# Kernel tuning notes

Hardware: AMD Instinct MI355X
Metric: run time of the kernel (lower is better)

The kernel has to match this reference:

```python
import jax, jax.numpy as jnp
import numpy as np

NUM_HEADS = 8
DIM = 192  # target_dim = min(channels_list)
CHANNELS = [192, 384, 768]
SIZES = [(32, 32), (16, 16), (8, 8)]
BATCH = 4


def conv1x1(x, w, b):
    # x: [B,C,H,W], w: [O,C,1,1], b: [O]
    y = jnp.einsum('bchw,oc->bohw', x, w[:, :, 0, 0])
    return y + b[None, :, None, None]


def cross_attention(x, ctx, wq, wkv, wp, bp):
    # x: [B,N,C] queries, ctx: [B,M,C] key/value source
    B, N, C = x.shape
    M = ctx.shape[1]
    h = NUM_HEADS
    d = C // h
    scale = d ** -0.5
    q = (x @ wq.T).reshape(B, N, h, d).transpose(0, 2, 1, 3)          # [B,h,N,d]
    kv = ctx @ wkv.T                                                   # [B,M,2C]
    k = kv[..., :C].reshape(B, M, h, d).transpose(0, 2, 1, 3)          # [B,h,M,d]
    v = kv[..., C:].reshape(B, M, h, d).transpose(0, 2, 1, 3)          # [B,h,M,d]
    attn = jax.nn.softmax(jnp.einsum('bhnd,bhmd->bhnm', q, k) * scale, axis=-1)
    o = jnp.einsum('bhnm,bhmd->bhnd', attn, v)
    o = o.transpose(0, 2, 1, 3).reshape(B, N, C)
    return o @ wp.T + bp


def setup_inputs() -> dict:
    key = jax.random.key(0)
    ks = iter(jax.random.split(key, 64))
    s = 0.02
    inp = {}
    for i, (c, (H, W)) in enumerate(zip(CHANNELS, SIZES)):
        inp[f'f{i}'] = jax.random.normal(next(ks), (BATCH, c, H, W), dtype=jnp.float32)
    # input projections (scale 0 has c == target_dim -> Identity, no params)
    for i in (1, 2):
        c = CHANNELS[i]
        inp[f'proj{i}_w'] = jax.random.normal(next(ks), (DIM, c, 1, 1), dtype=jnp.float32) * s
        inp[f'proj{i}_b'] = jnp.zeros((DIM,), dtype=jnp.float32)
    # cross-attention params per scale (qkv_bias=False; proj has bias)
    for i in range(3):
        inp[f'q{i}_w'] = jax.random.normal(next(ks), (DIM, DIM), dtype=jnp.float32) * s
        inp[f'kv{i}_w'] = jax.random.normal(next(ks), (2 * DIM, DIM), dtype=jnp.float32) * s
        inp[f'pr{i}_w'] = jax.random.normal(next(ks), (DIM, DIM), dtype=jnp.float32) * s
        inp[f'pr{i}_b'] = jnp.zeros((DIM,), dtype=jnp.float32)
    # output projections back to each channel count
    for i, c in enumerate(CHANNELS):
        inp[f'out{i}_w'] = jax.random.normal(next(ks), (c, DIM, 1, 1), dtype=jnp.float32) * s
        inp[f'out{i}_b'] = jnp.zeros((c,), dtype=jnp.float32)
    return inp


def _forward(f0, f1, f2,
             proj1_w, proj1_b, proj2_w, proj2_b,
             q0_w, kv0_w, pr0_w, pr0_b,
             q1_w, kv1_w, pr1_w, pr1_b,
             q2_w, kv2_w, pr2_w, pr2_b,
             out0_w, out0_b, out1_w, out1_b, out2_w, out2_b):
    projected = [
        f0,  # Identity (channels == target_dim)
        conv1x1(f1, proj1_w, proj1_b),
        conv1x1(f2, proj2_w, proj2_b),
    ]
    attn_params = [
        (q0_w, kv0_w, pr0_w, pr0_b),
        (q1_w, kv1_w, pr1_w, pr1_b),
        (q2_w, kv2_w, pr2_w, pr2_b),
    ]
    out_params = [(out0_w, out0_b), (out1_w, out1_b), (out2_w, out2_b)]
    outputs = []
    for i in range(3):
        feat = projected[i]
        B, C, H, W = feat.shape
        x = feat.reshape(B, C, H * W).transpose(0, 2, 1)  # [B,N,C]
        ctxs = []
        for j in range(3):
            if j != i:
                r = jax.image.resize(projected[j], (B, C, H, W), method='bilinear', antialias=False)
                ctxs.append(r.reshape(B, C, H * W).transpose(0, 2, 1))
        ctx = jnp.concatenate(ctxs, axis=1)  # [B,M,C]
        enh = cross_attention(x, ctx, *attn_params[i])
        enh = enh.transpose(0, 2, 1).reshape(B, C, H, W) + feat
        outputs.append(conv1x1(enh, *out_params[i]))
    return tuple(outputs)


def reference(f0, f1, f2,
              proj1_w, proj1_b, proj2_w, proj2_b,
              q0_w, kv0_w, pr0_w, pr0_b,
              q1_w, kv1_w, pr1_w, pr1_b,
              q2_w, kv2_w, pr2_w, pr2_b,
              out0_w, out0_b, out1_w, out1_b, out2_w, out2_b):
    return _forward(f0, f1, f2,
                    proj1_w, proj1_b, proj2_w, proj2_b,
                    q0_w, kv0_w, pr0_w, pr0_b,
                    q1_w, kv1_w, pr1_w, pr1_b,
                    q2_w, kv2_w, pr2_w, pr2_b,
                    out0_w, out0_b, out1_w, out1_b, out2_w, out2_b)
```

## Files before the change

kernel.cpp:

```cpp
#include <hip/hip_runtime.h>
#include <math.h>

#define BB 4
#define DIM 192
#define HEADS 8
#define HD 24

typedef __attribute__((ext_vector_type(8))) short short8v;
typedef __attribute__((ext_vector_type(4))) short short4v;
typedef __attribute__((ext_vector_type(4))) float f32x4;
typedef __attribute__((ext_vector_type(4))) unsigned uint4v;

__device__ __forceinline__ short f2bf(float f) {
  unsigned u = __builtin_bit_cast(unsigned, f);
  u += 0x7FFF + ((u >> 16) & 1);
  return (short)(u >> 16);
}
__device__ __forceinline__ unsigned pk2(float a, float b) {
  return (unsigned)(unsigned short)f2bf(a) | ((unsigned)(unsigned short)f2bf(b) << 16);
}
__device__ __forceinline__ float bf2f(unsigned u16) {
  return __builtin_bit_cast(float, u16 << 16);
}
__device__ __forceinline__ void gl_lds16(const void* g, void* l) {
  __builtin_amdgcn_global_load_lds(
      (const __attribute__((address_space(1))) unsigned int*)g,
      (__attribute__((address_space(3))) unsigned int*)l, 16, 0, 0);
}
__device__ __forceinline__ int xcd_swz(int bid, int nwg) {
  int q = nwg >> 3, r = nwg & 7;
  int xcd = bid & 7, idx = bid >> 3;
  return (xcd < r) ? (xcd * (q + 1) + idx) : (r * (q + 1) + (xcd - r) * q + idx);
}

struct PJob {
  int type;
  const float* s0; const float* s1; const float* s2;
  void* dst;
  int P0, P1v;
  int t_begin, t_end;
};
struct PJobs { PJob j[20]; };

__global__ __launch_bounds__(256) void prep_k(PJobs jobs, int nj) {
  int tid = blockIdx.x * 256 + threadIdx.x;
  for (int ji = 0; ji < 20; ++ji) {
    if (ji >= nj) return;
    PJob g = jobs.j[ji];
    if (tid < g.t_begin || tid >= g.t_end) continue;
    int t = tid - g.t_begin;
    if (g.type == 0) {
      float4 v = *(const float4*)&g.s0[(size_t)t * 4];
      uint2 u = {pk2(v.x, v.y), pk2(v.z, v.w)};
      *(uint2*)&((short*)g.dst)[(size_t)t * 4] = u;
    } else if (g.type == 1) {
      int X = g.P0, C = g.P1v, C8 = C >> 3;
      int x = t % X, c8 = (t / X) % C8, b = t / (X * C8);
      const float* s = g.s0 + ((size_t)b * C + c8 * 8) * X + x;
      unsigned h[8];
#pragma unroll
      for (int j = 0; j < 8; ++j) h[j] = (unsigned)(unsigned short)f2bf(s[(size_t)j * X]);
      uint4 u = {h[0] | (h[1] << 16), h[2] | (h[3] << 16), h[4] | (h[5] << 16), h[6] | (h[7] << 16)};
      *(uint4*)&((short*)g.dst)[((size_t)b * X + x) * C + c8 * 8] = u;
    } else if (g.type == 2) {
      int o = t;
      const float* w = g.s0 + (size_t)o * 192;
      float acc = g.s2[o];
      for (int k = 0; k < 192; ++k) acc += w[k] * g.s1[k];
      ((float*)g.dst)[o] = acc;
    } else {
      int c4 = t % 48, o = t / 48;
      const float* w = g.s0 + (size_t)o * 192;
      float a0 = 0, a1 = 0, a2 = 0, a3 = 0;
      for (int k = 0; k < 192; ++k) {
        float wv = w[k];
        float4 pv = *(const float4*)&g.s1[(size_t)k * 192 + c4 * 4];
        a0 += wv * pv.x; a1 += wv * pv.y; a2 += wv * pv.z; a3 += wv * pv.w;
      }
      uint2 u = {pk2(a0, a1), pk2(a2, a3)};
      *(uint2*)&((short*)g.dst)[(size_t)o * 192 + c4 * 4] = u;
    }
    return;
  }
}

struct MJob {
  const short* A; const short* W; const float* bias; const float* T;
  void* out;
  int K, nOT, mode, tokPerB;
  float scale;
  int blk_begin, blk_end;
};
struct MJobs { MJob j[10]; };

__global__ __launch_bounds__(256) void mgemm_k(MJobs jobs, int nj, int nwg) {
  __shared__ short Asl[64 * 192];
  __shared__ short Wsl[64 * 192];
  int blk = xcd_swz(blockIdx.x, nwg);
  for (int ji = 0; ji < 10; ++ji) {
    if (ji >= nj) return;
    MJob g = jobs.j[ji];
    if (blk < g.blk_begin || blk >= g.blk_end) continue;
    int lb = blk - g.blk_begin;
    int ot = lb % g.nOT, tt = lb / g.nOT;
    int t0 = tt * 64, o0 = ot * 64;
    int tid = threadIdx.x, wv = tid >> 6, lane = tid & 63, c = lane & 15, qi = lane >> 4;
    const int K = g.K;
    int rowK[6];
#pragma unroll
    for (int i = 0; i < 6; ++i) {
      int o16 = i * 256 + tid;
      int row = o16 / 24, ch = o16 - row * 24;
      rowK[i] = row * K + ((ch ^ (row & 7)) << 3);
    }
    const short* Ab = g.A + (size_t)t0 * K;
    const short* Wb = g.W + (size_t)o0 * K;
    f32x4 acc[4];
#pragma unroll
    for (int jj = 0; jj < 4; ++jj) acc[jj] = (f32x4){0.f, 0.f, 0.f, 0.f};
    int nkc = K / 192;
    int swz = c & 7;
    for (int kc = 0; kc < nkc; ++kc) {
      if (kc) __syncthreads();
      int kco = kc * 192;
#pragma unroll
      for (int i = 0; i < 6; ++i) gl_lds16(Ab + rowK[i] + kco, &Asl[(i * 256 + wv * 64) * 8]);
#pragma unroll
      for (int i = 0; i < 6; ++i) gl_lds16(Wb + rowK[i] + kco, &Wsl[(i * 256 + wv * 64) * 8]);
      asm volatile("s_waitcnt vmcnt(0)" ::: "memory");
      __syncthreads();
      const short* Lb = (g.mode == 0) ? Wsl : Asl;
      const short* Rb = (g.mode == 0) ? Asl : Wsl;
      int lrow = wv * 16 + c;
#pragma unroll
      for (int ks = 0; ks < 6; ++ks) {
        int chx = ((ks * 4 + qi) ^ swz) << 3;
        short8v lf = *(const short8v*)&Lb[lrow * 192 + chx];
#pragma unroll
        for (int jj = 0; jj < 4; ++jj) {
          short8v rf = *(const short8v*)&Rb[(jj * 16 + c) * 192 + chx];
          acc[jj] = __builtin_amdgcn_mfma_f32_16x16x32_bf16(lf, rf, acc[jj], 0, 0, 0);
        }
      }
    }
    int OST = g.nOT * 64;
    if (g.mode == 0) {
      int ob = o0 + wv * 16 + (qi << 2);
      float4 bv = {0.f, 0.f, 0.f, 0.f};
      if (g.bias) bv = *(const float4*)&g.bias[ob];
      float s = g.scale;
      short* op = (short*)g.out;
#pragma unroll
      for (int jj = 0; jj < 4; ++jj) {
        size_t tok = t0 + jj * 16 + c;
        uint2 u = {pk2(acc[jj][0] * s + bv.x, acc[jj][1] * s + bv.y),
                   pk2(acc[jj][2] * s + bv.z, acc[jj][3] * s + bv.w)};
        *(uint2*)&op[tok * OST + ob] = u;
      }
    } else {
      int tokb = t0 + wv * 16;
      int b = tokb / g.tokPerB;
      int nl = tokb - b * g.tokPerB + (qi << 2);
#pragma unroll
      for (int jj = 0; jj < 4; ++jj) {
        int o = o0 + jj * 16 + c;
        size_t idx = ((size_t)b * OST + o) * g.tokPerB + nl;
        if (g.mode == 1) {
          uint2 u = {pk2(acc[jj][0], acc[jj][1]), pk2(acc[jj][2], acc[jj][3])};
          *(uint2*)&((short*)g.out)[idx] = u;
        } else if (g.mode == 2) {
          float4 tv = *(const float4*)&g.T[idx];
          float4 ov = {acc[jj][0] + tv.x, acc[jj][1] + tv.y, acc[jj][2] + tv.z, acc[jj][3] + tv.w};
          *(float4*)&((float*)g.out)[idx] = ov;
        } else {
          float bvv = g.bias ? g.bias[o] : 0.f;
          float4 ov = {acc[jj][0] + bvv, acc[jj][1] + bvv, acc[jj][2] + bvv, acc[jj][3] + bvv};
          *(float4*)&((float*)g.out)[idx] = ov;
        }
      }
    }
    return;
  }
}

struct RJob {
  const short* src;
  short* dst;
  int Hs, Ws, Wd, Mtot;
  float ry, rx;
  int t_begin, t_end;
};
struct RJobs { RJob j[6]; };

__global__ __launch_bounds__(256) void resize_k(RJobs jobs) {
  int tid = blockIdx.x * 256 + threadIdx.x;
  for (int ji = 0; ji < 6; ++ji) {
    RJob g = jobs.j[ji];
    if (tid < g.t_begin || tid >= g.t_end) continue;
    int t = tid - g.t_begin;
    int c8 = t % 24;
    int rest = t / 24;
    int HWd = g.Wd * g.Wd;
    int n = rest % HWd, b = rest / HWd;
    int y = n / g.Wd, x = n % g.Wd;
    float fy = (y + 0.5f) * g.ry - 0.5f;
    float fx = (x + 0.5f) * g.rx - 0.5f;
    int y0 = (int)floorf(fy), x0 = (int)floorf(fx);
    float wy = fy - (float)y0, wx = fx - (float)x0;
    int Hs = g.Hs, Ws = g.Ws;
    int y0c = min(max(y0, 0), Hs - 1), y1c = min(max(y0 + 1, 0), Hs - 1);
    int x0c = min(max(x0, 0), Ws - 1), x1c = min(max(x0 + 1, 0), Ws - 1);
    size_t sb = (size_t)b * Hs * Ws;
    const short* sp = g.src;
    uint4 u00 = *(const uint4*)&sp[(sb + y0c * Ws + x0c) * 192 + c8 * 8];
    uint4 u01 = *(const uint4*)&sp[(sb + y0c * Ws + x1c) * 192 + c8 * 8];
    uint4 u10 = *(const uint4*)&sp[(sb + y1c * Ws + x0c) * 192 + c8 * 8];
    uint4 u11 = *(const uint4*)&sp[(sb + y1c * Ws + x1c) * 192 + c8 * 8];
    float w00 = (1.f - wy) * (1.f - wx), w01 = (1.f - wy) * wx;
    float w10 = wy * (1.f - wx), w11 = wy * wx;
    unsigned a[4], bq[4], cq[4], dq[4];
    a[0]=u00.x; a[1]=u00.y; a[2]=u00.z; a[3]=u00.w;
    bq[0]=u01.x; bq[1]=u01.y; bq[2]=u01.z; bq[3]=u01.w;
    cq[0]=u10.x; cq[1]=u10.y; cq[2]=u10.z; cq[3]=u10.w;
    dq[0]=u11.x; dq[1]=u11.y; dq[2]=u11.z; dq[3]=u11.w;
    unsigned r[4];
#pragma unroll
    for (int k = 0; k < 4; ++k) {
      float lo = w00 * bf2f(a[k] & 0xffff) + w01 * bf2f(bq[k] & 0xffff) +
                 w10 * bf2f(cq[k] & 0xffff) + w11 * bf2f(dq[k] & 0xffff);
      float hi = w00 * bf2f(a[k] >> 16) + w01 * bf2f(bq[k] >> 16) +
                 w10 * bf2f(cq[k] >> 16) + w11 * bf2f(dq[k] >> 16);
      r[k] = pk2(lo, hi);
    }
    uint4 u = {r[0], r[1], r[2], r[3]};
    *(uint4*)&g.dst[((size_t)b * g.Mtot + n) * 192 + c8 * 8] = u;
    return;
  }
}

struct AJob {
  const short* q;
  const short* K;
  const short* V;
  short* o;
  int N, M;
  int blk_begin, blk_end;
};
struct AJobs { AJob j[3]; };

__global__ __launch_bounds__(256) void attn_k(AJobs jobs, int cpx) {
  __shared__ __align__(16) short LDSbuf[2][7432];
  int bid = blockIdx.x;
  int blk = (bid & 7) * cpx + (bid >> 3);
  int tidx = threadIdx.x;
  if (tidx < 4) {
    ((int*)LDSbuf[0])[1536 + tidx] = 0;
    ((int*)LDSbuf[1])[1536 + tidx] = 0;
  }
  if (tidx < 64) {
    ((int*)LDSbuf[0])[3172 + tidx] = 0x3F803F80;
    ((int*)LDSbuf[1])[3172 + tidx] = 0x3F803F80;
  }
  for (int ji = 0; ji < 3; ++ji) {
    AJob g = jobs.j[ji];
    if (blk < g.blk_begin || blk >= g.blk_end) continue;
    int lb = blk - g.blk_begin;
    const int N = g.N, M = g.M;
    int nch = N >> 6;
    int bh = lb / nch, ct = lb % nch;
    int b = bh >> 3, h = bh & 7;
    int wv = tidx >> 6, lane = tidx & 63;
    int c = lane & 15, qi = lane >> 4;
    int nw0 = (ct << 6) + (wv << 4);

    const short* Kg = g.K + (size_t)b * M * 192 + h * 24;
    const short* Vg = g.V + ((size_t)b * 192 + h * 24) * M;

    const short* gp[4];
    int gstr[4], loff[4];
    bool val[4];
#pragma unroll
    for (int i = 0; i < 4; ++i) {
      int s = tidx + (i << 8);
      val[i] = (s < 792);
      if (s < 384) {
        int row = s / 3, part = s - row * 3;
        gp[i] = Kg + row * 192 + part * 8;
        gstr[i] = 128 * 192;
        loff[i] = s * 8;
      } else {
        int v = s - 384;
        int row = v / 17, col = v - row * 17;
        int colc = (col < 16) ? col : 0;
        gp[i] = val[i] ? (Vg + (size_t)row * M + colc * 8) : Vg;
        gstr[i] = 128;
        loff[i] = 3080 + v * 8;
      }
    }

    short8v qf = *(const short8v*)&g.q[((size_t)b * N + nw0 + c) * 192 + h * 24 + (qi << 3)];
    if (qi == 3) {
#pragma unroll
      for (int j = 0; j < 8; ++j) qf[j] = 0;
    }

    f32x4 of0 = {0.f, 0.f, 0.f, 0.f}, of1 = {0.f, 0.f, 0.f, 0.f};
    const f32x4 zf = {0.f, 0.f, 0.f, 0.f};

#pragma unroll
    for (int i = 0; i < 4; ++i)
      if (val[i]) { gl_lds16(gp[i], &LDSbuf[0][loff[i]]); gp[i] += gstr[i]; }

    int nt = M >> 7;
    int cur = 0;
    for (int t = 0; t < nt; ++t) {
      asm volatile("s_waitcnt vmcnt(0)" ::: "memory");
      __syncthreads();
      if (t + 1 < nt) {
#pragma unroll
        for (int i = 0; i < 4; ++i)
          if (val[i]) { gl_lds16(gp[i], &LDSbuf[cur ^ 1][loff[i]]); gp[i] += gstr[i]; }
      }
      const short* Kl = LDSbuf[cur];
      const short* Vl = LDSbuf[cur] + 3080;
      f32x4 sr[8];
#pragma unroll
      for (int jj = 0; jj < 8; ++jj) {
        short8v kb = *(const short8v*)&Kl[(c + 16 * jj) * 24 + (qi << 3)];
        sr[jj] = __builtin_amdgcn_mfma_f32_16x16x32_bf16(kb, qf, zf, 0, 0, 0);
      }
      unsigned pk[8][2];
#pragma unroll
      for (int jj = 0; jj < 8; ++jj) {
        pk[jj][0] = pk2(__expf(sr[jj][0]), __expf(sr[jj][1]));
        pk[jj][1] = pk2(__expf(sr[jj][2]), __expf(sr[jj][3]));
      }
#pragma unroll
      for (int ks = 0; ks < 4; ++ks) {
        uint4v pu = {pk[2 * ks][0], pk[2 * ks][1], pk[2 * ks + 1][0], pk[2 * ks + 1][1]};
        short8v pa = __builtin_bit_cast(short8v, pu);
        int vb0 = c * 136 + ks * 32 + (qi << 2);
        int vb1 = (16 + c) * 136 + ks * 32 + (qi << 2);
        short4v l0 = *(const short4v*)&Vl[vb0];
        short4v h0 = *(const short4v*)&Vl[vb0 + 16];
        short4v l1 = *(const short4v*)&Vl[vb1];
        short4v h1 = *(const short4v*)&Vl[vb1 + 16];
        short8v v0, v1;
#pragma unroll
        for (int j2 = 0; j2 < 4; ++j2) {
          v0[j2] = l0[j2]; v0[4 + j2] = h0[j2];
          v1[j2] = l1[j2]; v1[4 + j2] = h1[j2];
        }
        of0 = __builtin_amdgcn_mfma_f32_16x16x32_bf16(pa, v0, of0, 0, 0, 0);
        of1 = __builtin_amdgcn_mfma_f32_16x16x32_bf16(pa, v1, of1, 0, 0, 0);
      }
      cur ^= 1;
    }
    float ls[4];
#pragma unroll
    for (int r = 0; r < 4; ++r) ls[r] = __shfl(of1[r], (qi << 4) + 8);
#pragma unroll
    for (int r = 0; r < 4; ++r) {
      float inv = 1.f / ls[r];
      int n = nw0 + (qi << 2) + r;
      short* op = g.o + ((size_t)b * N + n) * 192 + h * 24;
      op[c] = f2bf(of0[r] * inv);
      if (c < 8) op[16 + c] = f2bf(of1[r] * inv);
    }
    return;
  }
}

extern "C" void kernel_launch(void* const* d_in, const int* in_sizes, int n_in,
                              void* d_out, int out_size, void* d_ws, size_t ws_size,
                              hipStream_t stream) {
  (void)in_sizes; (void)n_in; (void)out_size; (void)ws_size;
  const float* f0 = (const float*)d_in[0];
  const float* f1 = (const float*)d_in[1];
  const float* f2 = (const float*)d_in[2];
  const float* p1w = (const float*)d_in[3];
  const float* p1b = (const float*)d_in[4];
  const float* p2w = (const float*)d_in[5];
  const float* p2b = (const float*)d_in[6];
  const float* qw[3]  = {(const float*)d_in[7],  (const float*)d_in[11], (const float*)d_in[15]};
  const float* kvw[3] = {(const float*)d_in[8],  (const float*)d_in[12], (const float*)d_in[16]};
  const float* prw[3] = {(const float*)d_in[9],  (const float*)d_in[13], (const float*)d_in[17]};
  const float* prb[3] = {(const float*)d_in[10], (const float*)d_in[14], (const float*)d_in[18]};
  const float* ow[3]  = {(const float*)d_in[19], (const float*)d_in[21], (const float*)d_in[23]};
  const float* ob[3]  = {(const float*)d_in[20], (const float*)d_in[22], (const float*)d_in[24]};

  char* ws = (char*)d_ws;
  short* x0    = (short*)(ws + 0);
  short* x1in  = (short*)(ws + 1572864);
  short* x2in  = (short*)(ws + 2359296);
  short* P1    = (short*)(ws + 2752512);
  short* P2    = (short*)(ws + 3145728);
  short* ctx0  = (short*)(ws + 3244032);
  short* ctx1  = (short*)(ws + 6389760);
  short* ctx2  = (short*)(ws + 7176192);
  short* qb    = (short*)(ws + 7372800);
  short* Kb    = (short*)(ws + 9437184);
  short* Vb    = (short*)(ws + 13565952);
  short* attb  = (short*)(ws + 17694720);
  float* T0    = (float*)(ws + 19759104);
  float* T1    = (float*)(ws + 22904832);
  float* T2    = (float*)(ws + 24477696);
  short* W2b   = (short*)(ws + 25264128);
  short* wcvt  = (short*)(ws + 25780224);
  float* bfin  = (float*)(ws + 27402240);

  short* p1w_b = wcvt;
  short* p2w_b = wcvt + 73728;
  short* qw_b[3]  = {wcvt + 221184, wcvt + 258048, wcvt + 294912};
  short* kvw_b[3] = {wcvt + 331776, wcvt + 405504, wcvt + 479232};
  short* ow_b[3]  = {wcvt + 552960, wcvt + 589824, wcvt + 663552};
  short* W2_b[3]  = {W2b, W2b + 36864, W2b + 110592};
  short* qs[3]  = {qb, qb + 786432, qb + 983040};
  short* Ks[3]  = {Kb, Kb + 1572864, Kb + 1966080};
  short* Vs[3]  = {Vb, Vb + 1572864, Vb + 1966080};
  short* atts[3] = {attb, attb + 786432, attb + 983040};
  float* out0 = (float*)d_out;
  float* outp[3] = {out0, out0 + 786432, out0 + 1179648};

  const int Ns[3] = {1024, 256, 64};
  const int Ms[3] = {2048, 512, 128};
  const float qsc = 0.20412414523193154f;

  {
    PJobs js{};
    int t0 = 0, n = 0;
    auto add = [&](PJob j, int tc) { j.t_begin = t0; j.t_end = t0 + tc; js.j[n++] = j; t0 += tc; };
    add({0, p1w, nullptr, nullptr, p1w_b, 0, 0, 0, 0}, 18432);
    add({0, p2w, nullptr, nullptr, p2w_b, 0, 0, 0, 0}, 36864);
    for (int i = 0; i < 3; ++i) add({0, qw[i], nullptr, nullptr, qw_b[i], 0, 0, 0, 0}, 9216);
    for (int i = 0; i < 3; ++i) add({0, kvw[i], nullptr, nullptr, kvw_b[i], 0, 0, 0, 0}, 18432);
    add({0, ow[0], nullptr, nullptr, ow_b[0], 0, 0, 0, 0}, 9216);
    add({0, ow[1], nullptr, nullptr, ow_b[1], 0, 0, 0, 0}, 18432);
    add({0, ow[2], nullptr, nullptr, ow_b[2], 0, 0, 0, 0}, 36864);
    add({1, f0, nullptr, nullptr, x0, 1024, 192, 0, 0}, 98304);
    add({1, f1, nullptr, nullptr, x1in, 256, 384, 0, 0}, 49152);
    add({1, f2, nullptr, nullptr, x2in, 64, 768, 0, 0}, 24576);
    add({2, ow[0], prb[0], ob[0], bfin, 0, 0, 0, 0}, 192);
    add({2, ow[1], prb[1], ob[1], bfin + 192, 0, 0, 0, 0}, 384);
    add({2, ow[2], prb[2], ob[2], bfin + 576, 0, 0, 0, 0}, 768);
    add({3, ow[0], prw[0], nullptr, W2_b[0], 0, 0, 0, 0}, 9216);
    add({3, ow[1], prw[1], nullptr, W2_b[1], 0, 0, 0, 0}, 18432);
    add({3, ow[2], prw[2], nullptr, W2_b[2], 0, 0, 0, 0}, 36864);
    hipLaunchKernelGGL(prep_k, dim3((t0 + 255) / 256), dim3(256), 0, stream, js, n);
  }
  {
    MJobs js{};
    int b0 = 0, n = 0;
    auto add = [&](MJob j, int nb) { j.blk_begin = b0; j.blk_end = b0 + nb; js.j[n++] = j; b0 += nb; };
    add({x1in, p1w_b, p1b, nullptr, P1, 384, 3, 0, 0, 1.f, 0, 0}, 16 * 3);
    add({x2in, p2w_b, p2b, nullptr, P2, 768, 3, 0, 0, 1.f, 0, 0}, 4 * 3);
    add({x0, qw_b[0], nullptr, nullptr, qs[0], 192, 3, 0, 0, qsc, 0, 0}, 64 * 3);
    add({x0, ow_b[0], bfin, nullptr, T0, 192, 3, 3, 1024, 1.f, 0, 0}, 64 * 3);
    hipLaunchKernelGGL(mgemm_k, dim3(b0), dim3(256), 0, stream, js, n, b0);
  }
  {
    RJobs js{};
    int t0 = 0, n = 0;
    auto add = [&](RJob j, int tc) { j.t_begin = t0; j.t_end = t0 + tc; js.j[n++] = j; t0 += tc; };
    add({P1, ctx0, 16, 16, 32, 2048, 0.5f, 0.5f, 0, 0}, 98304);
    add({P2, ctx0 + 1024 * 192, 8, 8, 32, 2048, 0.25f, 0.25f, 0, 0}, 98304);
    add({x0, ctx1, 32, 32, 16, 512, 2.f, 2.f, 0, 0}, 24576);
    add({P2, ctx1 + 256 * 192, 8, 8, 16, 512, 0.5f, 0.5f, 0, 0}, 24576);
    add({x0, ctx2, 32, 32, 8, 128, 4.f, 4.f, 0, 0}, 6144);
    add({P1, ctx2 + 64 * 192, 16, 16, 8, 128, 2.f, 2.f, 0, 0}, 6144);
    hipLaunchKernelGGL(resize_k, dim3(t0 / 256), dim3(256), 0, stream, js);
  }
  {
    MJobs js{};
    int b0 = 0, n = 0;
    auto add = [&](MJob j, int nb) { j.blk_begin = b0; j.blk_end = b0 + nb; js.j[n++] = j; b0 += nb; };
    add({P1, qw_b[1], nullptr, nullptr, qs[1], 192, 3, 0, 0, qsc, 0, 0}, 16 * 3);
    add({P2, qw_b[2], nullptr, nullptr, qs[2], 192, 3, 0, 0, qsc, 0, 0}, 4 * 3);
    add({ctx0, kvw_b[0], nullptr, nullptr, Ks[0], 192, 3, 0, 0, 1.f, 0, 0}, 128 * 3);
    add({ctx1, kvw_b[1], nullptr, nullptr, Ks[1], 192, 3, 0, 0, 1.f, 0, 0}, 32 * 3);
    add({ctx2, kvw_b[2], nullptr, nullptr, Ks[2], 192, 3, 0, 0, 1.f, 0, 0}, 8 * 3);
    add({ctx0, kvw_b[0] + 36864, nullptr, nullptr, Vs[0], 192, 3, 1, 2048, 1.f, 0, 0}, 128 * 3);
    add({ctx1, kvw_b[1] + 36864, nullptr, nullptr, Vs[1], 192, 3, 1, 512, 1.f, 0, 0}, 32 * 3);
    add({ctx2, kvw_b[2] + 36864, nullptr, nullptr, Vs[2], 192, 3, 1, 128, 1.f, 0, 0}, 8 * 3);
    add({P1, ow_b[1], bfin + 192, nullptr, T1, 192, 6, 3, 256, 1.f, 0, 0}, 16 * 6);
    add({P2, ow_b[2], bfin + 576, nullptr, T2, 192, 12, 3, 64, 1.f, 0, 0}, 4 * 12);
    hipLaunchKernelGGL(mgemm_k, dim3(b0), dim3(256), 0, stream, js, n, b0);
  }
  {
    AJobs js{};
    int b0 = 0;
    for (int i = 0; i < 3; ++i) {
      int nb = BB * HEADS * (Ns[i] / 64);
      js.j[i] = {qs[i], Ks[i], Vs[i], atts[i], Ns[i], Ms[i], b0, b0 + nb};
      b0 += nb;
    }
    hipLaunchKernelGGL(attn_k, dim3(b0), dim3(256), 0, stream, js, b0 / 8);
  }
  {
    MJobs js{};
    int b0 = 0, n = 0;
    auto add = [&](MJob j, int nb) { j.blk_begin = b0; j.blk_end = b0 + nb; js.j[n++] = j; b0 += nb; };
    add({atts[0], W2_b[0], nullptr, T0, outp[0], 192, 3, 2, 1024, 1.f, 0, 0}, 64 * 3);
    add({atts[1], W2_b[1], nullptr, T1, outp[1], 192, 6, 2, 256, 1.f, 0, 0}, 16 * 6);
    add({atts[2], W2_b[2], nullptr, T2, outp[2], 192, 12, 2, 64, 1.f, 0, 0}, 4 * 12);
    hipLaunchKernelGGL(mgemm_k, dim3(b0), dim3(256), 0, stream, js, n, b0);
  }
}
```

Baseline: 89.52 us.

## Triple-buffer attention loads, pre-permute V layout, and fold weight product into MFMA GEMM

The attention kernel moves from double to triple buffering. It waits with a partial vmcnt so two tiles stay in flight, and it raises wave priority around the MFMA sections. The V output in mode 1 is written with a permuted token order, so attention can load each V fragment with one 16-byte LDS read instead of two 8-byte reads plus a shuffle. The fused out-projection times proj-weight product now runs as a bf16 MFMA GEMM job after transposing prw in prep, replacing the scalar fp32 loop. This adds a third LDS buffer, which may lower occupancy, and the weight product is now computed from bf16 inputs.

```diff
diff --git a/kernel.cpp b/kernel.cpp
--- a/kernel.cpp
+++ b/kernel.cpp
@@ -62,23 +62,12 @@
       for (int j = 0; j < 8; ++j) h[j] = (unsigned)(unsigned short)f2bf(s[(size_t)j * X]);
       uint4 u = {h[0] | (h[1] << 16), h[2] | (h[3] << 16), h[4] | (h[5] << 16), h[6] | (h[7] << 16)};
       *(uint4*)&((short*)g.dst)[((size_t)b * X + x) * C + c8 * 8] = u;
-    } else if (g.type == 2) {
+    } else {
       int o = t;
       const float* w = g.s0 + (size_t)o * 192;
       float acc = g.s2[o];
       for (int k = 0; k < 192; ++k) acc += w[k] * g.s1[k];
       ((float*)g.dst)[o] = acc;
-    } else {
-      int c4 = t % 48, o = t / 48;
-      const float* w = g.s0 + (size_t)o * 192;
-      float a0 = 0, a1 = 0, a2 = 0, a3 = 0;
-      for (int k = 0; k < 192; ++k) {
-        float wv = w[k];
-        float4 pv = *(const float4*)&g.s1[(size_t)k * 192 + c4 * 4];
-        a0 += wv * pv.x; a1 += wv * pv.y; a2 += wv * pv.z; a3 += wv * pv.w;
-      }
-      uint2 u = {pk2(a0, a1), pk2(a2, a3)};
-      *(uint2*)&((short*)g.dst)[(size_t)o * 192 + c4 * 4] = u;
     }
     return;
   }
@@ -164,15 +153,18 @@
 #pragma unroll
       for (int jj = 0; jj < 4; ++jj) {
         int o = o0 + jj * 16 + c;
-        size_t idx = ((size_t)b * OST + o) * g.tokPerB + nl;
         if (g.mode == 1) {
+          int np = (nl & ~31) + 8 * ((nl >> 2) & 3) + 4 * ((nl >> 4) & 1);
+          size_t idx = ((size_t)b * OST + o) * g.tokPerB + np;
           uint2 u = {pk2(acc[jj][0], acc[jj][1]), pk2(acc[jj][2], acc[jj][3])};
           *(uint2*)&((short*)g.out)[idx] = u;
         } else if (g.mode == 2) {
+          size_t idx = ((size_t)b * OST + o) * g.tokPerB + nl;
           float4 tv = *(const float4*)&g.T[idx];
           float4 ov = {acc[jj][0] + tv.x, acc[jj][1] + tv.y, acc[jj][2] + tv.z, acc[jj][3] + tv.w};
           *(float4*)&((float*)g.out)[idx] = ov;
         } else {
+          size_t idx = ((size_t)b * OST + o) * g.tokPerB + nl;
           float bvv = g.bias ? g.bias[o] : 0.f;
           float4 ov = {acc[jj][0] + bvv, acc[jj][1] + bvv, acc[jj][2] + bvv, acc[jj][3] + bvv};
           *(float4*)&((float*)g.out)[idx] = ov;
@@ -248,18 +240,21 @@
 };
 struct AJobs { AJob j[3]; };
 
-__global__ __launch_bounds__(256) void attn_k(AJobs jobs, int cpx) {
-  __shared__ __align__(16) short LDSbuf[2][7432];
+#define ABUF 7432
+#define VBASE 3080
+
+__global__ __launch_bounds__(256, 3) void attn_k(AJobs jobs, int cpx) {
+  __shared__ __align__(16) short LDSbuf[3][ABUF];
   int bid = blockIdx.x;
   int blk = (bid & 7) * cpx + (bid >> 3);
   int tidx = threadIdx.x;
-  if (tidx < 4) {
-    ((int*)LDSbuf[0])[1536 + tidx] = 0;
-    ((int*)LDSbuf[1])[1536 + tidx] = 0;
-  }
   if (tidx < 64) {
-    ((int*)LDSbuf[0])[3172 + tidx] = 0x3F803F80;
-    ((int*)LDSbuf[1])[3172 + tidx] = 0x3F803F80;
+#pragma unroll
+    for (int bb = 0; bb < 3; ++bb)
+      ((int*)&LDSbuf[bb][VBASE + 24 * 136])[tidx] = 0x3F803F80;
+  } else if (tidx < 76) {
+    int bb = (tidx - 64) >> 2, e = (tidx - 64) & 3;
+    ((int*)&LDSbuf[bb][3072])[e] = 0;
   }
   for (int ji = 0; ji < 3; ++ji) {
     AJob g = jobs.j[ji];
@@ -294,7 +289,7 @@
         int colc = (col < 16) ? col : 0;
         gp[i] = val[i] ? (Vg + (size_t)row * M + colc * 8) : Vg;
         gstr[i] = 128;
-        loff[i] = 3080 + v * 8;
+        loff[i] = VBASE + v * 8;
       }
     }
 
@@ -307,54 +302,53 @@
     f32x4 of0 = {0.f, 0.f, 0.f, 0.f}, of1 = {0.f, 0.f, 0.f, 0.f};
     const f32x4 zf = {0.f, 0.f, 0.f, 0.f};
 
+    int nt = M >> 7;
 #pragma unroll
     for (int i = 0; i < 4; ++i)
       if (val[i]) { gl_lds16(gp[i], &LDSbuf[0][loff[i]]); gp[i] += gstr[i]; }
-
-    int nt = M >> 7;
-    int cur = 0;
+    if (nt > 1) {
+#pragma unroll
+      for (int i = 0; i < 4; ++i)
+        if (val[i]) { gl_lds16(gp[i], &LDSbuf[1][loff[i]]); gp[i] += gstr[i]; }
+    }
+
     for (int t = 0; t < nt; ++t) {
-      asm volatile("s_waitcnt vmcnt(0)" ::: "memory");
-      __syncthreads();
-      if (t + 1 < nt) {
+      if (t + 1 < nt) asm volatile("s_waitcnt vmcnt(3) lgkmcnt(0)" ::: "memory");
+      else            asm volatile("s_waitcnt vmcnt(0) lgkmcnt(0)" ::: "memory");
+      __builtin_amdgcn_s_barrier();
+      if (t + 2 < nt) {
+        short* dst = LDSbuf[(t + 2) % 3];
 #pragma unroll
         for (int i = 0; i < 4; ++i)
-          if (val[i]) { gl_lds16(gp[i], &LDSbuf[cur ^ 1][loff[i]]); gp[i] += gstr[i]; }
-      }
-      const short* Kl = LDSbuf[cur];
-      const short* Vl = LDSbuf[cur] + 3080;
+          if (val[i]) { gl_lds16(gp[i], &dst[loff[i]]); gp[i] += gstr[i]; }
+      }
+      const short* Kl = LDSbuf[t % 3];
+      const short* Vl = Kl + VBASE;
+      __builtin_amdgcn_s_setprio(1);
       f32x4 sr[8];
 #pragma unroll
       for (int jj = 0; jj < 8; ++jj) {
         short8v kb = *(const short8v*)&Kl[(c + 16 * jj) * 24 + (qi << 3)];
         sr[jj] = __builtin_amdgcn_mfma_f32_16x16x32_bf16(kb, qf, zf, 0, 0, 0);
       }
+      __builtin_amdgcn_s_setprio(0);
       unsigned pk[8][2];
 #pragma unroll
       for (int jj = 0; jj < 8; ++jj) {
         pk[jj][0] = pk2(__expf(sr[jj][0]), __expf(sr[jj][1]));
         pk[jj][1] = pk2(__expf(sr[jj][2]), __expf(sr[jj][3]));
       }
+      __builtin_amdgcn_s_setprio(1);
 #pragma unroll
       for (int ks = 0; ks < 4; ++ks) {
         uint4v pu = {pk[2 * ks][0], pk[2 * ks][1], pk[2 * ks + 1][0], pk[2 * ks + 1][1]};
         short8v pa = __builtin_bit_cast(short8v, pu);
-        int vb0 = c * 136 + ks * 32 + (qi << 2);
-        int vb1 = (16 + c) * 136 + ks * 32 + (qi << 2);
-        short4v l0 = *(const short4v*)&Vl[vb0];
-        short4v h0 = *(const short4v*)&Vl[vb0 + 16];
-        short4v l1 = *(const short4v*)&Vl[vb1];
-        short4v h1 = *(const short4v*)&Vl[vb1 + 16];
-        short8v v0, v1;
-#pragma unroll
-        for (int j2 = 0; j2 < 4; ++j2) {
-          v0[j2] = l0[j2]; v0[4 + j2] = h0[j2];
-          v1[j2] = l1[j2]; v1[4 + j2] = h1[j2];
-        }
+        short8v v0 = *(const short8v*)&Vl[c * 136 + ks * 32 + (qi << 3)];
+        short8v v1 = *(const short8v*)&Vl[(16 + c) * 136 + ks * 32 + (qi << 3)];
         of0 = __builtin_amdgcn_mfma_f32_16x16x32_bf16(pa, v0, of0, 0, 0, 0);
         of1 = __builtin_amdgcn_mfma_f32_16x16x32_bf16(pa, v1, of1, 0, 0, 0);
       }
-      cur ^= 1;
+      __builtin_amdgcn_s_setprio(0);
     }
     float ls[4];
 #pragma unroll
@@ -408,12 +402,14 @@
   short* W2b   = (short*)(ws + 25264128);
   short* wcvt  = (short*)(ws + 25780224);
   float* bfin  = (float*)(ws + 27402240);
+  short* prwT  = (short*)(ws + 27407616);
 
   short* p1w_b = wcvt;
   short* p2w_b = wcvt + 73728;
   short* qw_b[3]  = {wcvt + 221184, wcvt + 258048, wcvt + 294912};
   short* kvw_b[3] = {wcvt + 331776, wcvt + 405504, wcvt + 479232};
   short* ow_b[3]  = {wcvt + 552960, wcvt + 589824, wcvt + 663552};
+  short* prwT_b[3] = {prwT, prwT + 36864, prwT + 73728};
   short* W2_b[3]  = {W2b, W2b + 36864, W2b + 110592};
   short* qs[3]  = {qb, qb + 786432, qb + 983040};
   short* Ks[3]  = {Kb, Kb + 1572864, Kb + 1966080};
@@ -424,6 +420,7 @@
 
   const int Ns[3] = {1024, 256, 64};
   const int Ms[3] = {2048, 512, 128};
+  const int Couts[3] = {192, 384, 768};
   const float qsc = 0.20412414523193154f;
 
   {
@@ -440,12 +437,11 @@
     add({1, f0, nullptr, nullptr, x0, 1024, 192, 0, 0}, 98304);
     add({1, f1, nullptr, nullptr, x1in, 256, 384, 0, 0}, 49152);
     add({1, f2, nullptr, nullptr, x2in, 64, 768, 0, 0}, 24576);
+    for (int i = 0; i < 3; ++i)
+      add({1, prw[i], nullptr, nullptr, prwT_b[i], 192, 192, 0, 0}, 4608);
     add({2, ow[0], prb[0], ob[0], bfin, 0, 0, 0, 0}, 192);
     add({2, ow[1], prb[1], ob[1], bfin + 192, 0, 0, 0, 0}, 384);
     add({2, ow[2], prb[2], ob[2], bfin + 576, 0, 0, 0, 0}, 768);
-    add({3, ow[0], prw[0], nullptr, W2_b[0], 0, 0, 0, 0}, 9216);
-    add({3, ow[1], prw[1], nullptr, W2_b[1], 0, 0, 0, 0}, 18432);
-    add({3, ow[2], prw[2], nullptr, W2_b[2], 0, 0, 0, 0}, 36864);
     hipLaunchKernelGGL(prep_k, dim3((t0 + 255) / 256), dim3(256), 0, stream, js, n);
   }
   {
@@ -456,6 +452,9 @@
     add({x2in, p2w_b, p2b, nullptr, P2, 768, 3, 0, 0, 1.f, 0, 0}, 4 * 3);
     add({x0, qw_b[0], nullptr, nullptr, qs[0], 192, 3, 0, 0, qsc, 0, 0}, 64 * 3);
     add({x0, ow_b[0], bfin, nullptr, T0, 192, 3, 3, 1024, 1.f, 0, 0}, 64 * 3);
+    for (int i = 0; i < 3; ++i)
+      add({ow_b[i], prwT_b[i], nullptr, nullptr, W2_b[i], 192, 3, 0, 0, 1.f, 0, 0},
+          (Couts[i] / 64) * 3);
     hipLaunchKernelGGL(mgemm_k, dim3(b0), dim3(256), 0, stream, js, n, b0);
   }
   {
```

Measured after the change: 81.34 us. 9.1% less time.
